# Kernel optimization log

Measured on AMD Instinct MI355X. Metric: run time of the kernel, lower is better.

## Reference

```python
import math
import jax, jax.numpy as jnp
import numpy as np

DIM = 3
NB = 8  # 2**DIM blades, grade-sorted: [1, e1, e2, e3, e12, e13, e23, e123]
GRADE_SLICES = [(0, 1), (1, 4), (4, 7), (7, 8)]
SUBSPACES = [1, 3, 3, 1]
GRADE_IDX = np.repeat(np.arange(4), SUBSPACES)  # blade -> grade index
EPS = 1e-6
SQRT2 = math.sqrt(2.0)


def _build_cayley():
    # Cl(3,0) Euclidean Cayley table, blades sorted by (grade, bitmask).
    masks = sorted(range(NB), key=lambda m: (bin(m).count("1"), m))
    pos = {m: i for i, m in enumerate(masks)}
    cay = np.zeros((NB, NB, NB), dtype=np.float32)
    for i, mi in enumerate(masks):
        for k, mk in enumerate(masks):
            a, s = mi >> 1, 0
            while a:
                s += bin(a & mk).count("1")
                a >>= 1
            cay[i, pos[mi ^ mk], k] = -1.0 if (s & 1) else 1.0
    triples = []
    for gi in range(4):
        for gj in range(4):
            for gk in range(4):
                (i0, i1), (j0, j1), (k0, k1) = GRADE_SLICES[gi], GRADE_SLICES[gj], GRADE_SLICES[gk]
                if np.any(cay[i0:i1, j0:j1, k0:k1] != 0):
                    triples.append((gi, gj, gk))
    return cay, triples

CAYLEY_NP, TRIPLES = _build_cayley()
NPATHS = len(TRIPLES)  # 20 nonzero grade-triple paths for Cl(3,0)


def mv_linear(x, w, b=None):
    # x: [B,n,8]; w: [m,n,4] (one weight per grade subspace); bias -> scalar blade only.
    w8 = w[..., GRADE_IDX]  # [m,n,8]
    out = jnp.einsum("bni,mni->bmi", x, w8)
    if b is not None:
        out = out.at[..., 0].add(b)
    return out


def grade_q(x):
    # per-grade squared magnitude (Euclidean metric -> all blade signs +1): [B,n,8]->[B,n,4]
    return jnp.stack([jnp.sum(x[..., s:e] ** 2, axis=-1) for s, e in GRADE_SLICES], axis=-1)


def normalization(x, a):
    # CGENN NormalizationLayer (init=0): interpolate per-grade norm toward 1 via sigmoid gate.
    norms = jnp.sqrt(grade_q(x))  # [B,n,4]
    sa = jax.nn.sigmoid(a)  # [n,4]
    norms = sa[None] * (norms - 1.0) + 1.0
    return x / (norms[..., GRADE_IDX] + EPS)


def mv_silu(x, a, b):
    # MVSiLU with invariant='mag2': gate on [scalar, q_grade1, q_grade2, q_grade3].
    q = grade_q(x)  # [B,n,4]
    inv = jnp.concatenate([x[..., :1], q[..., 1:]], axis=-1)  # [B,n,4]
    gate = a[None] * inv + b[None]
    return jax.nn.sigmoid(gate[..., GRADE_IDX]) * x


def fc_geometric_product(x, xr, w, cayley):
    # out[b,m,j] = sum_{n,i,k} x[b,n,i] * cayley[i,j,k] * W[m,n,path(gi,gj,gk)] * xr[b,n,k]
    B, n = x.shape[0], x.shape[1]
    m = w.shape[0]
    out = jnp.zeros((B, m, NB), dtype=x.dtype)
    for t, (gi, gj, gk) in enumerate(TRIPLES):
        (i0, i1), (j0, j1), (k0, k1) = GRADE_SLICES[gi], GRADE_SLICES[gj], GRADE_SLICES[gk]
        tmp = jnp.einsum("bni,ijk,bnk->bnj", x[..., i0:i1], cayley[i0:i1, j0:j1, k0:k1], xr[..., k0:k1])
        out = out.at[:, :, j0:j1].add(jnp.einsum("bnj,mn->bmj", tmp, w[:, :, t]))
    return out


def cw_geometric_product(x, xr, w, cayley):
    # channel-wise steerable GP: out[b,n,j] = sum_{i,k} x[b,n,i]*cayley[i,j,k]*w[n,path]*xr[b,n,k]
    out = jnp.zeros_like(x)
    for t, (gi, gj, gk) in enumerate(TRIPLES):
        (i0, i1), (j0, j1), (k0, k1) = GRADE_SLICES[gi], GRADE_SLICES[gj], GRADE_SLICES[gk]
        tmp = jnp.einsum("bni,ijk,bnk->bnj", x[..., i0:i1], cayley[i0:i1, j0:j1, k0:k1], xr[..., k0:k1])
        out = out.at[:, :, j0:j1].add(tmp * w[None, :, t, None])
    return out


B, IN, HID, OUT = 1024, 256, 512, 128


def setup_inputs():
    key = jax.random.key(0)
    ks = jax.random.split(key, 16)

    def nrm(k, shape, std):
        return jax.random.normal(k, shape, dtype=jnp.float32) * std

    s_in = 1.0 / math.sqrt(IN)
    s_hid = 1.0 / math.sqrt(HID)
    return {
        "x": jax.random.normal(ks[0], (B, IN, NB), dtype=jnp.float32),
        "lr1_w": nrm(ks[1], (IN, IN, 4), s_in),
        "n1_a": jnp.zeros((IN, 4), jnp.float32),
        "ll1_w": nrm(ks[2], (HID, IN, 4), s_in),
        "ll1_b": jnp.zeros((HID,), jnp.float32),
        "w1": nrm(ks[3], (HID, IN, NPATHS), 1.0 / math.sqrt(IN * (DIM + 1))),
        "act_a": jnp.ones((HID, 4), jnp.float32),
        "act_b": jnp.zeros((HID, 4), jnp.float32),
        "lrg_w": nrm(ks[4], (HID, HID, 4), s_hid),
        "ng_a": jnp.zeros((HID, 4), jnp.float32),
        "llg_w": nrm(ks[5], (HID, HID, 4), s_hid),
        "llg_b": jnp.zeros((HID,), jnp.float32),
        "wg": nrm(ks[6], (HID, NPATHS), 1.0 / math.sqrt(DIM + 1)),
        "lr2_w": nrm(ks[7], (HID, HID, 4), s_hid),
        "n2_a": jnp.zeros((HID, 4), jnp.float32),
        "ll2_w": nrm(ks[8], (OUT, HID, 4), s_hid),
        "ll2_b": jnp.zeros((OUT,), jnp.float32),
        "w2": nrm(ks[9], (OUT, HID, NPATHS), 1.0 / math.sqrt(HID * (DIM + 1))),
    }


def reference(x, lr1_w, n1_a, ll1_w, ll1_b, w1, act_a, act_b,
              lrg_w, ng_a, llg_w, llg_b, wg,
              lr2_w, n2_a, ll2_w, ll2_b, w2):
    cayley = jnp.asarray(CAYLEY_NP)
    # fcgp1: right linear -> normalize -> weighted geometric product + first-order term
    xr = normalization(mv_linear(x, lr1_w), n1_a)
    h = (mv_linear(x, ll1_w, ll1_b) + fc_geometric_product(x, xr, w1, cayley)) / SQRT2
    h = mv_silu(h, act_a, act_b)
    # channel-wise steerable geometric product layer
    hr = normalization(mv_linear(h, lrg_w), ng_a)
    h = (mv_linear(h, llg_w, llg_b) + cw_geometric_product(h, hr, wg, cayley)) / SQRT2
    h = mv_silu(h, act_a, act_b)
    # fcgp2
    hr = normalization(mv_linear(h, lr2_w), n2_a)
    out = (mv_linear(h, ll2_w, ll2_b) + fc_geometric_product(h, hr, w2, cayley)) / SQRT2
    return out
```

## Files before the change

kernel.cpp:

```cpp
#include <hip/hip_runtime.h>
#include <math.h>


typedef unsigned short u16;
typedef __attribute__((ext_vector_type(8))) short short8;
typedef __attribute__((ext_vector_type(4))) float f32x4;

#define RSQRT2F 0.70710678118654752440f

__device__ inline void gl_lds16(const void* g, void* l) {
  __builtin_amdgcn_global_load_lds(
      (const __attribute__((address_space(1))) void*)g,
      (__attribute__((address_space(3))) void*)l, 16, 0, 0);
}

__device__ constexpr int PP_I[64] = {
  0,0,0,0,0,0,0,0,  1,1,1,1,1,1,1,1,  2,2,2,2,2,2,2,2,  3,3,3,3,3,3,3,3,
  4,4,4,4,4,4,4,4,  5,5,5,5,5,5,5,5,  6,6,6,6,6,6,6,6,  7,7,7,7,7,7,7,7};
__device__ constexpr int PP_K[64] = {
  0,1,2,3,4,5,6,7,  0,1,2,3,4,5,6,7,  0,1,2,3,4,5,6,7,  0,1,2,3,4,5,6,7,
  0,1,2,3,4,5,6,7,  0,1,2,3,4,5,6,7,  0,1,2,3,4,5,6,7,  0,1,2,3,4,5,6,7};
__device__ constexpr int PP_C[64] = {
   0, 1, 2, 3, 4, 5, 6, 7,
   9, 8,15,16,13,14,21,20,
  10,15, 8,17,12,21,14,19,
  11,16,17, 8,21,12,13,18,
  29,24,23,35,22,34,33,28,
  30,25,35,23,34,22,32,27,
  31,35,25,24,33,32,22,26,
  43,42,41,40,39,38,37,36};
__device__ constexpr int PP_T[64] = {
   0, 1, 1, 1, 2, 2, 2, 3,
   5, 4, 7, 7, 6, 6, 9, 8,
   5, 7, 4, 7, 6, 9, 6, 8,
   5, 7, 7, 4, 9, 6, 6, 8,
  13,11,11,15,10,14,14,12,
  13,11,15,11,14,10,14,12,
  13,15,11,11,14,14,10,12,
  19,18,18,18,17,17,17,16};
__device__ constexpr int PP_J[64] = {
  0,1,2,3,4,5,6,7,
  1,0,4,5,2,3,7,6,
  2,4,0,6,1,7,3,5,
  3,5,6,0,7,1,2,4,
  4,2,1,7,0,6,5,3,
  5,3,7,1,6,0,4,2,
  6,7,3,2,5,4,0,1,
  7,6,5,4,3,2,1,0};
__device__ constexpr float PP_S[64] = {
  1, 1, 1, 1, 1, 1, 1, 1,
  1, 1, 1, 1, 1, 1, 1, 1,
  1,-1, 1, 1,-1,-1, 1,-1,
  1,-1,-1, 1, 1,-1,-1, 1,
  1,-1, 1, 1,-1,-1, 1,-1,
  1,-1,-1, 1, 1,-1,-1, 1,
  1, 1,-1, 1,-1, 1,-1,-1,
  1, 1,-1, 1,-1, 1,-1,-1};

__device__ constexpr int GJ_CNT[8] = {4,6,6,6,6,6,6,4};
__device__ constexpr int GJ_C[8][6] = {
  {0,8,22,36,0,0},
  {1,9,12,23,26,37},
  {2,10,13,24,27,38},
  {3,11,14,25,28,39},
  {4,15,18,29,32,40},
  {5,16,19,30,33,41},
  {6,17,20,31,34,42},
  {7,21,35,43,0,0}};
__device__ constexpr int GJ_T[8][6] = {
  {0,4,10,16,0,0},
  {1,5,6,11,12,17},
  {1,5,6,11,12,17},
  {1,5,6,11,12,17},
  {2,7,8,13,14,18},
  {2,7,8,13,14,18},
  {2,7,8,13,14,18},
  {3,9,15,19,0,0}};
__device__ constexpr int GRADE[8] = {0,1,1,1,2,2,2,3};

__device__ inline float sigm(float x) { return 1.0f / (1.0f + expf(-x)); }
__device__ inline u16 f2bf(float f) {
  unsigned u = __float_as_uint(f);
  return (u16)((u + 0x7fffu + ((u >> 16) & 1u)) >> 16);
}
__device__ inline float bf2f(u16 h) { return __uint_as_float(((unsigned)h) << 16); }

#define BT 128
#define MT 128
#define BKc 64

__global__ __launch_bounds__(256) void mfma_gemm(
    const u16* __restrict__ Alin, const u16* __restrict__ Pfeat,
    const u16* __restrict__ WLin, const u16* __restrict__ WLin2,
    const u16* __restrict__ WGp,
    float* __restrict__ out1, float* __restrict__ out2,
    int N, int M, int aug, int planeA, int planeO, int KSbits, int KCbits)
{
  const int zz    = blockIdx.z;
  const int set   = zz >> (3 + KSbits);
  const int rem   = zz & ((8 << KSbits) - 1);
  const int j     = rem >> KSbits;
  const int slice = rem & ((1 << KSbits) - 1);
  const u16* WL   = set ? WLin2 : WLin;
  float* outp     = set ? out2 : out1;

  const int b0   = blockIdx.y * BT;
  const int m0   = blockIdx.x * MT;
  const int tid  = threadIdx.x;
  const int lane = tid & 63;
  const int wave = tid >> 6;
  const int wr   = wave >> 1;
  const int wc   = wave & 1;
  const int l15  = lane & 15;
  const int lq   = lane >> 4;

  __shared__ u16 As[BT * BKc];
  __shared__ u16 Bs[MT * BKc];

  f32x4 zero = {0.f, 0.f, 0.f, 0.f};
  f32x4 acc[4][4];
  #pragma unroll
  for (int r = 0; r < 4; ++r)
    #pragma unroll
    for (int c = 0; c < 4; ++c) acc[r][c] = zero;

  const int g = GRADE[j];
  const int npass = aug ? (1 + GJ_CNT[j]) : 1;
  const int KC = 1 << KCbits;
  const int cper = (npass << KCbits) >> KSbits;
  const int cbeg = slice * cper;

  const int srow = lane >> 3;
  const int sslot = lane & 7;

  for (int ci = cbeg; ci < cbeg + cper; ++ci) {
    const int p  = ci >> KCbits;
    const int k0 = (ci & (KC - 1)) << 6;
    const u16* Abase = (p == 0) ? Alin + (size_t)j * planeA
                                : Pfeat + (size_t)GJ_C[j][p - 1] * planeA;
    const u16* Wbase = (p == 0) ? WL + (size_t)g * M * N
                                : WGp + (size_t)GJ_T[j][p - 1] * M * N;
    const u16* Asrc = Abase + (size_t)b0 * N + k0;
    const u16* Bsrc = Wbase + (size_t)m0 * N + k0;

    __syncthreads();
    #pragma unroll
    for (int q = 0; q < 4; ++q) {
      int inst = wave * 4 + q;
      int row  = inst * 8 + srow;
      int kg   = sslot ^ (row & 7);
      gl_lds16(Asrc + (size_t)row * N + kg * 8, &As[inst * 512]);
    }
    #pragma unroll
    for (int q = 0; q < 4; ++q) {
      int inst = wave * 4 + q;
      int row  = inst * 8 + srow;
      int kg   = sslot ^ (row & 7);
      gl_lds16(Bsrc + (size_t)row * N + kg * 8, &Bs[inst * 512]);
    }
    __syncthreads();

    #pragma unroll
    for (int s = 0; s < 2; ++s) {
      const int kq = s * 4 + lq;
      short8 af[4], bfr[4];
      #pragma unroll
      for (int r = 0; r < 4; ++r) {
        int row = wr * 64 + r * 16 + l15;
        af[r] = *(const short8*)(&As[row * BKc + (kq ^ (row & 7)) * 8]);
      }
      #pragma unroll
      for (int c = 0; c < 4; ++c) {
        int row = wc * 64 + c * 16 + l15;
        bfr[c] = *(const short8*)(&Bs[row * BKc + (kq ^ (row & 7)) * 8]);
      }
      #pragma unroll
      for (int r = 0; r < 4; ++r)
        #pragma unroll
        for (int c = 0; c < 4; ++c)
          acc[r][c] = __builtin_amdgcn_mfma_f32_16x16x32_bf16(af[r], bfr[c], acc[r][c], 0, 0, 0);
    }
  }

  float* obase = outp + (size_t)(slice * 8 + j) * planeO;
  #pragma unroll
  for (int r = 0; r < 4; ++r)
    #pragma unroll
    for (int c = 0; c < 4; ++c)
      #pragma unroll
      for (int e = 0; e < 4; ++e) {
        int bb = b0 + wr * 64 + r * 16 + lq * 4 + e;
        int mm = m0 + wc * 64 + c * 16 + l15;
        obase[(size_t)bb * M + mm] = acc[r][c][e];
      }
}

struct RepackDesc { const float* in; u16* out; int MN; int S; };
struct RepackArgs { RepackDesc d[8]; const float* x; u16* xp; int PS; };

__global__ void repack_all(RepackArgs a)
{
  int mn = blockIdx.x * 256 + threadIdx.x;
  if (blockIdx.y == 8) {
    if (mn >= a.PS) return;
    float v[8];
    *(float4*)(v)     = *(const float4*)(a.x + (size_t)mn * 8);
    *(float4*)(v + 4) = *(const float4*)(a.x + (size_t)mn * 8 + 4);
    #pragma unroll
    for (int jj = 0; jj < 8; ++jj) a.xp[(size_t)jj * a.PS + mn] = f2bf(v[jj]);
    return;
  }
  RepackDesc d = a.d[blockIdx.y];
  if (mn >= d.MN) return;
  if (d.S == 4) {
    float4 v = ((const float4*)d.in)[mn];
    d.out[(size_t)0 * d.MN + mn] = f2bf(v.x);
    d.out[(size_t)1 * d.MN + mn] = f2bf(v.y);
    d.out[(size_t)2 * d.MN + mn] = f2bf(v.z);
    d.out[(size_t)3 * d.MN + mn] = f2bf(v.w);
  } else {
    #pragma unroll
    for (int q = 0; q < 5; ++q) {
      float4 v = *(const float4*)(d.in + (size_t)mn * 20 + q * 4);
      d.out[(size_t)(q * 4 + 0) * d.MN + mn] = f2bf(v.x);
      d.out[(size_t)(q * 4 + 1) * d.MN + mn] = f2bf(v.y);
      d.out[(size_t)(q * 4 + 2) * d.MN + mn] = f2bf(v.z);
      d.out[(size_t)(q * 4 + 3) * d.MN + mn] = f2bf(v.w);
    }
  }
}

__global__ void pair_norm_p(const u16* __restrict__ up, const float* __restrict__ vpart,
                            const float* __restrict__ na, u16* __restrict__ Pp,
                            int PS, int M, int KS)
{
  int t = blockIdx.x * 256 + threadIdx.x;
  if (t >= PS) return;
  int m = t % M;
  float u[8], v[8];
  #pragma unroll
  for (int jj = 0; jj < 8; ++jj) {
    u[jj] = bf2f(up[(size_t)jj * PS + t]);
    float s = 0.f;
    for (int sl = 0; sl < KS; ++sl) s += vpart[(size_t)(sl * 8 + jj) * PS + t];
    v[jj] = s;
  }
  float q[4];
  q[0] = sqrtf(v[0] * v[0]);
  q[1] = sqrtf(v[1] * v[1] + v[2] * v[2] + v[3] * v[3]);
  q[2] = sqrtf(v[4] * v[4] + v[5] * v[5] + v[6] * v[6]);
  q[3] = sqrtf(v[7] * v[7]);
  float sc[4];
  #pragma unroll
  for (int gg = 0; gg < 4; ++gg) {
    float sa = sigm(na[m * 4 + gg]);
    sc[gg] = 1.0f / (sa * (q[gg] - 1.0f) + 1.0f + 1e-6f);
  }
  #pragma unroll
  for (int jj = 0; jj < 8; ++jj) v[jj] *= sc[GRADE[jj]];
  float p[44];
  #pragma unroll
  for (int c = 0; c < 44; ++c) p[c] = 0.f;
  #pragma unroll
  for (int e = 0; e < 64; ++e)
    p[PP_C[e]] += PP_S[e] * u[PP_I[e]] * v[PP_K[e]];
  #pragma unroll
  for (int c = 0; c < 44; ++c) Pp[(size_t)c * PS + t] = f2bf(p[c]);
}

__global__ void bias_silu_p(const float* __restrict__ hpart, const float* __restrict__ bias,
                            const float* __restrict__ ga, const float* __restrict__ gb,
                            u16* __restrict__ sh, int PS, int M, int KS)
{
  int t = blockIdx.x * 256 + threadIdx.x;
  if (t >= PS) return;
  int m = t % M;
  float v[8];
  #pragma unroll
  for (int jj = 0; jj < 8; ++jj) {
    float s = 0.f;
    for (int sl = 0; sl < KS; ++sl) s += hpart[(size_t)(sl * 8 + jj) * PS + t];
    v[jj] = s;
  }
  v[0] += bias[m];
  #pragma unroll
  for (int jj = 0; jj < 8; ++jj) v[jj] *= RSQRT2F;
  float inv[4];
  inv[0] = v[0];
  inv[1] = v[1]*v[1] + v[2]*v[2] + v[3]*v[3];
  inv[2] = v[4]*v[4] + v[5]*v[5] + v[6]*v[6];
  inv[3] = v[7]*v[7];
  float gt[4];
  #pragma unroll
  for (int gg = 0; gg < 4; ++gg)
    gt[gg] = sigm(ga[m * 4 + gg] * inv[gg] + gb[m * 4 + gg]);
  #pragma unroll
  for (int jj = 0; jj < 8; ++jj)
    sh[(size_t)jj * PS + t] = f2bf(v[jj] * gt[GRADE[jj]]);
}

__global__ void cw_silu_p(const float* __restrict__ llg, const u16* __restrict__ up,
                          const float* __restrict__ hrraw, const float* __restrict__ na,
                          const float* __restrict__ wg, const float* __restrict__ bias,
                          const float* __restrict__ ga, const float* __restrict__ gb,
                          u16* __restrict__ sh, int PS, int M)
{
  int t = blockIdx.x * 256 + threadIdx.x;
  if (t >= PS) return;
  int n = t % M;
  float acc[8], u[8], v[8], w[20];
  #pragma unroll
  for (int jj = 0; jj < 8; ++jj) {
    acc[jj] = llg[(size_t)jj * PS + t];
    u[jj]   = bf2f(up[(size_t)jj * PS + t]);
    v[jj]   = hrraw[(size_t)jj * PS + t];
  }
  float q[4];
  q[0] = sqrtf(v[0] * v[0]);
  q[1] = sqrtf(v[1] * v[1] + v[2] * v[2] + v[3] * v[3]);
  q[2] = sqrtf(v[4] * v[4] + v[5] * v[5] + v[6] * v[6]);
  q[3] = sqrtf(v[7] * v[7]);
  float sc[4];
  #pragma unroll
  for (int gg = 0; gg < 4; ++gg) {
    float sa = sigm(na[n * 4 + gg]);
    sc[gg] = 1.0f / (sa * (q[gg] - 1.0f) + 1.0f + 1e-6f);
  }
  #pragma unroll
  for (int jj = 0; jj < 8; ++jj) v[jj] *= sc[GRADE[jj]];
  #pragma unroll
  for (int qq = 0; qq < 5; ++qq)
    *(float4*)(w + qq * 4) = *(const float4*)(wg + (size_t)n * 20 + qq * 4);
  acc[0] += bias[n];
  #pragma unroll
  for (int e = 0; e < 64; ++e)
    acc[PP_J[e]] += PP_S[e] * u[PP_I[e]] * v[PP_K[e]] * w[PP_T[e]];
  #pragma unroll
  for (int jj = 0; jj < 8; ++jj) acc[jj] *= RSQRT2F;
  float inv[4];
  inv[0] = acc[0];
  inv[1] = acc[1]*acc[1] + acc[2]*acc[2] + acc[3]*acc[3];
  inv[2] = acc[4]*acc[4] + acc[5]*acc[5] + acc[6]*acc[6];
  inv[3] = acc[7]*acc[7];
  float gt[4];
  #pragma unroll
  for (int gg = 0; gg < 4; ++gg)
    gt[gg] = sigm(ga[n * 4 + gg] * inv[gg] + gb[n * 4 + gg]);
  #pragma unroll
  for (int jj = 0; jj < 8; ++jj)
    sh[(size_t)jj * PS + t] = f2bf(acc[jj] * gt[GRADE[jj]]);
}

__global__ void final_p(const float* __restrict__ pre, const float* __restrict__ bias,
                        float* __restrict__ outp, int PS, int M, int KS)
{
  int t = blockIdx.x * 256 + threadIdx.x;
  if (t >= PS) return;
  int m = t % M;
  float v[8];
  #pragma unroll
  for (int jj = 0; jj < 8; ++jj) {
    float s = 0.f;
    for (int sl = 0; sl < KS; ++sl) s += pre[(size_t)(sl * 8 + jj) * PS + t];
    v[jj] = s;
  }
  v[0] += bias[m];
  #pragma unroll
  for (int jj = 0; jj < 8; ++jj) v[jj] *= RSQRT2F;
  *(float4*)(outp + (size_t)t * 8)     = *(float4*)(v);
  *(float4*)(outp + (size_t)t * 8 + 4) = *(float4*)(v + 4);
}

extern "C" void kernel_launch(void* const* d_in, const int* in_sizes, int n_in,
                              void* d_out, int out_size, void* d_ws, size_t ws_size,
                              hipStream_t stream)
{
  const float* x     = (const float*)d_in[0];
  const float* lr1_w = (const float*)d_in[1];
  const float* n1_a  = (const float*)d_in[2];
  const float* ll1_w = (const float*)d_in[3];
  const float* ll1_b = (const float*)d_in[4];
  const float* w1    = (const float*)d_in[5];
  const float* act_a = (const float*)d_in[6];
  const float* act_b = (const float*)d_in[7];
  const float* lrg_w = (const float*)d_in[8];
  const float* ng_a  = (const float*)d_in[9];
  const float* llg_w = (const float*)d_in[10];
  const float* llg_b = (const float*)d_in[11];
  const float* wg    = (const float*)d_in[12];
  const float* lr2_w = (const float*)d_in[13];
  const float* n2_a  = (const float*)d_in[14];
  const float* ll2_w = (const float*)d_in[15];
  const float* ll2_b = (const float*)d_in[16];
  const float* w2    = (const float*)d_in[17];
  float* out = (float*)d_out;

  u16* W = (u16*)d_ws;
  size_t o = 0;
  u16* WL1  = W + o; o +=  262144;
  u16* WLL1 = W + o; o +=  524288;
  u16* WG1  = W + o; o += 2621440;
  u16* WLRG = W + o; o += 1048576;
  u16* WLLG = W + o; o += 1048576;
  u16* WLR2 = W + o; o += 1048576;
  u16* WLL2 = W + o; o +=  262144;
  u16* WG2  = W + o; o += 1310720;
  u16* XB   = W + o; o += 2097152;
  u16* HB   = W + o; o += 4194304;
  u16* P    = W + o; o += 23068672;
  float* f1 = (float*)(W + o);
  float* f2 = f1 + 8388608;
  float* hrP  = f2;
  float* llgP = f2 + 4194304;

  dim3 blk(256);
  const int PS1 = 1024 * 256, PS2 = 1024 * 512, PSO = 1024 * 128;

  RepackArgs ra = {{
    {lr1_w, WL1, 65536, 4}, {ll1_w, WLL1, 131072, 4}, {w1, WG1, 131072, 20},
    {lrg_w, WLRG, 262144, 4}, {llg_w, WLLG, 262144, 4}, {lr2_w, WLR2, 262144, 4},
    {ll2_w, WLL2, 65536, 4}, {w2, WG2, 65536, 20}},
    x, XB, PS1};
  repack_all<<<dim3(1024, 9), blk, 0, stream>>>(ra);

  mfma_gemm<<<dim3(2, 8, 16), blk, 0, stream>>>(XB, nullptr, WL1, nullptr, nullptr,
      f1, nullptr, 256, 256, 0, PS1, PS1, 1, 2);
  pair_norm_p<<<PS1 / 256, blk, 0, stream>>>(XB, f1, n1_a, P, PS1, 256, 2);
  mfma_gemm<<<dim3(4, 8, 16), blk, 0, stream>>>(XB, P, WLL1, nullptr, WG1,
      f1, nullptr, 256, 512, 1, PS1, PS2, 1, 2);
  bias_silu_p<<<PS2 / 256, blk, 0, stream>>>(f1, ll1_b, act_a, act_b, HB, PS2, 512, 2);

  mfma_gemm<<<dim3(4, 8, 16), blk, 0, stream>>>(HB, nullptr, WLRG, WLLG, nullptr,
      hrP, llgP, 512, 512, 0, PS2, PS2, 0, 3);
  cw_silu_p<<<PS2 / 256, blk, 0, stream>>>(llgP, HB, hrP, ng_a, wg, llg_b, act_a, act_b,
      HB, PS2, 512);

  mfma_gemm<<<dim3(4, 8, 16), blk, 0, stream>>>(HB, nullptr, WLR2, nullptr, nullptr,
      f1, nullptr, 512, 512, 0, PS2, PS2, 1, 3);
  pair_norm_p<<<PS2 / 256, blk, 0, stream>>>(HB, f1, n2_a, P, PS2, 512, 2);
  mfma_gemm<<<dim3(1, 8, 64), blk, 0, stream>>>(HB, P, WLL2, nullptr, WG2,
      f1, nullptr, 512, 128, 1, PS2, PSO, 3, 3);
  final_p<<<PSO / 256, blk, 0, stream>>>(f1, ll2_b, out, PSO, 128, 8);
}
```

Measured before the change: 261.8 us.

## Template GEMM tile shape and store intermediate partial sums in bf16

Templates the MFMA GEMM on block tile and wave layout, moving most launches to 256x128 tiles with four waves stacked along rows. The intermediate outputs (split-K partials, hr/llg projections) are now written as bf16 instead of fp32, and the consumer kernels convert them back. This halves the intermediate write and read traffic and improves reuse of weight tiles. In exchange, split-K partial sums are rounded to bf16 before being added, which loses precision, and the larger tiles mean fewer blocks and more registers per wave.

Result: slower. 268.4 us (+2.5%).

```diff
diff --git a/kernel.cpp b/kernel.cpp
--- a/kernel.cpp
+++ b/kernel.cpp
@@ -85,32 +85,36 @@
 }
 __device__ inline float bf2f(u16 h) { return __uint_as_float(((unsigned)h) << 16); }
 
-#define BT 128
-#define MT 128
 #define BKc 64
 
+template<int BT, int MT, int WR, int WC, int OUT16>
 __global__ __launch_bounds__(256) void mfma_gemm(
     const u16* __restrict__ Alin, const u16* __restrict__ Pfeat,
     const u16* __restrict__ WLin, const u16* __restrict__ WLin2,
     const u16* __restrict__ WGp,
-    float* __restrict__ out1, float* __restrict__ out2,
+    void* __restrict__ out1, void* __restrict__ out2,
     int N, int M, int aug, int planeA, int planeO, int KSbits, int KCbits)
 {
+  constexpr int FR = BT / 16 / WR;
+  constexpr int FC = MT / 16 / WC;
+  constexpr int AI = BT / 32;
+  constexpr int BI = MT / 32;
+
   const int zz    = blockIdx.z;
   const int set   = zz >> (3 + KSbits);
   const int rem   = zz & ((8 << KSbits) - 1);
   const int j     = rem >> KSbits;
   const int slice = rem & ((1 << KSbits) - 1);
   const u16* WL   = set ? WLin2 : WLin;
-  float* outp     = set ? out2 : out1;
+  void* outp      = set ? out2 : out1;
 
   const int b0   = blockIdx.y * BT;
   const int m0   = blockIdx.x * MT;
   const int tid  = threadIdx.x;
   const int lane = tid & 63;
   const int wave = tid >> 6;
-  const int wr   = wave >> 1;
-  const int wc   = wave & 1;
+  const int wr   = wave / WC;
+  const int wc   = wave % WC;
   const int l15  = lane & 15;
   const int lq   = lane >> 4;
 
@@ -118,11 +122,11 @@
   __shared__ u16 Bs[MT * BKc];
 
   f32x4 zero = {0.f, 0.f, 0.f, 0.f};
-  f32x4 acc[4][4];
-  #pragma unroll
-  for (int r = 0; r < 4; ++r)
-    #pragma unroll
-    for (int c = 0; c < 4; ++c) acc[r][c] = zero;
+  f32x4 acc[FR][FC];
+  #pragma unroll
+  for (int r = 0; r < FR; ++r)
+    #pragma unroll
+    for (int c = 0; c < FC; ++c) acc[r][c] = zero;
 
   const int g = GRADE[j];
   const int npass = aug ? (1 + GJ_CNT[j]) : 1;
@@ -130,7 +134,7 @@
   const int cper = (npass << KCbits) >> KSbits;
   const int cbeg = slice * cper;
 
-  const int srow = lane >> 3;
+  const int srow  = lane >> 3;
   const int sslot = lane & 7;
 
   for (int ci = cbeg; ci < cbeg + cper; ++ci) {
@@ -145,15 +149,15 @@
 
     __syncthreads();
     #pragma unroll
-    for (int q = 0; q < 4; ++q) {
-      int inst = wave * 4 + q;
+    for (int q = 0; q < AI; ++q) {
+      int inst = wave * AI + q;
       int row  = inst * 8 + srow;
       int kg   = sslot ^ (row & 7);
       gl_lds16(Asrc + (size_t)row * N + kg * 8, &As[inst * 512]);
     }
     #pragma unroll
-    for (int q = 0; q < 4; ++q) {
-      int inst = wave * 4 + q;
+    for (int q = 0; q < BI; ++q) {
+      int inst = wave * BI + q;
       int row  = inst * 8 + srow;
       int kg   = sslot ^ (row & 7);
       gl_lds16(Bsrc + (size_t)row * N + kg * 8, &Bs[inst * 512]);
@@ -163,35 +167,36 @@
     #pragma unroll
     for (int s = 0; s < 2; ++s) {
       const int kq = s * 4 + lq;
-      short8 af[4], bfr[4];
+      short8 af[FR], bfr[FC];
       #pragma unroll
-      for (int r = 0; r < 4; ++r) {
-        int row = wr * 64 + r * 16 + l15;
+      for (int r = 0; r < FR; ++r) {
+        int row = wr * (FR * 16) + r * 16 + l15;
         af[r] = *(const short8*)(&As[row * BKc + (kq ^ (row & 7)) * 8]);
       }
       #pragma unroll
-      for (int c = 0; c < 4; ++c) {
-        int row = wc * 64 + c * 16 + l15;
+      for (int c = 0; c < FC; ++c) {
+        int row = wc * (FC * 16) + c * 16 + l15;
         bfr[c] = *(const short8*)(&Bs[row * BKc + (kq ^ (row & 7)) * 8]);
       }
       #pragma unroll
-      for (int r = 0; r < 4; ++r)
+      for (int r = 0; r < FR; ++r)
         #pragma unroll
-        for (int c = 0; c < 4; ++c)
+        for (int c = 0; c < FC; ++c)
           acc[r][c] = __builtin_amdgcn_mfma_f32_16x16x32_bf16(af[r], bfr[c], acc[r][c], 0, 0, 0);
     }
   }
 
-  float* obase = outp + (size_t)(slice * 8 + j) * planeO;
-  #pragma unroll
-  for (int r = 0; r < 4; ++r)
-    #pragma unroll
-    for (int c = 0; c < 4; ++c)
+  const size_t po = (size_t)(slice * 8 + j) * planeO;
+  #pragma unroll
+  for (int r = 0; r < FR; ++r)
+    #pragma unroll
+    for (int c = 0; c < FC; ++c)
       #pragma unroll
       for (int e = 0; e < 4; ++e) {
-        int bb = b0 + wr * 64 + r * 16 + lq * 4 + e;
-        int mm = m0 + wc * 64 + c * 16 + l15;
-        obase[(size_t)bb * M + mm] = acc[r][c][e];
+        int bb = b0 + wr * (FR * 16) + r * 16 + lq * 4 + e;
+        int mm = m0 + wc * (FC * 16) + c * 16 + l15;
+        if (OUT16) ((u16*)outp)[po + (size_t)bb * M + mm] = f2bf(acc[r][c][e]);
+        else       ((float*)outp)[po + (size_t)bb * M + mm] = acc[r][c][e];
       }
 }
 
@@ -230,7 +235,7 @@
   }
 }
 
-__global__ void pair_norm_p(const u16* __restrict__ up, const float* __restrict__ vpart,
+__global__ void pair_norm_p(const u16* __restrict__ up, const u16* __restrict__ vpart,
                             const float* __restrict__ na, u16* __restrict__ Pp,
                             int PS, int M, int KS)
 {
@@ -242,7 +247,7 @@
   for (int jj = 0; jj < 8; ++jj) {
     u[jj] = bf2f(up[(size_t)jj * PS + t]);
     float s = 0.f;
-    for (int sl = 0; sl < KS; ++sl) s += vpart[(size_t)(sl * 8 + jj) * PS + t];
+    for (int sl = 0; sl < KS; ++sl) s += bf2f(vpart[(size_t)(sl * 8 + jj) * PS + t]);
     v[jj] = s;
   }
   float q[4];
@@ -268,7 +273,7 @@
   for (int c = 0; c < 44; ++c) Pp[(size_t)c * PS + t] = f2bf(p[c]);
 }
 
-__global__ void bias_silu_p(const float* __restrict__ hpart, const float* __restrict__ bias,
+__global__ void bias_silu_p(const u16* __restrict__ hpart, const float* __restrict__ bias,
                             const float* __restrict__ ga, const float* __restrict__ gb,
                             u16* __restrict__ sh, int PS, int M, int KS)
 {
@@ -279,7 +284,7 @@
   #pragma unroll
   for (int jj = 0; jj < 8; ++jj) {
     float s = 0.f;
-    for (int sl = 0; sl < KS; ++sl) s += hpart[(size_t)(sl * 8 + jj) * PS + t];
+    for (int sl = 0; sl < KS; ++sl) s += bf2f(hpart[(size_t)(sl * 8 + jj) * PS + t]);
     v[jj] = s;
   }
   v[0] += bias[m];
@@ -299,8 +304,8 @@
     sh[(size_t)jj * PS + t] = f2bf(v[jj] * gt[GRADE[jj]]);
 }
 
-__global__ void cw_silu_p(const float* __restrict__ llg, const u16* __restrict__ up,
-                          const float* __restrict__ hrraw, const float* __restrict__ na,
+__global__ void cw_silu_p(const u16* __restrict__ llg, const u16* __restrict__ up,
+                          const u16* __restrict__ hrraw, const float* __restrict__ na,
                           const float* __restrict__ wg, const float* __restrict__ bias,
                           const float* __restrict__ ga, const float* __restrict__ gb,
                           u16* __restrict__ sh, int PS, int M)
@@ -311,9 +316,9 @@
   float acc[8], u[8], v[8], w[20];
   #pragma unroll
   for (int jj = 0; jj < 8; ++jj) {
-    acc[jj] = llg[(size_t)jj * PS + t];
+    acc[jj] = bf2f(llg[(size_t)jj * PS + t]);
     u[jj]   = bf2f(up[(size_t)jj * PS + t]);
-    v[jj]   = hrraw[(size_t)jj * PS + t];
+    v[jj]   = bf2f(hrraw[(size_t)jj * PS + t]);
   }
   float q[4];
   q[0] = sqrtf(v[0] * v[0]);
@@ -408,10 +413,11 @@
   u16* XB   = W + o; o += 2097152;
   u16* HB   = W + o; o += 4194304;
   u16* P    = W + o; o += 23068672;
+  u16* PB16 = W + o; o += 8388608;
+  u16* HRG  = W + o; o += 8388608;
+  u16* hr16  = HRG;
+  u16* llg16 = HRG + 4194304;
   float* f1 = (float*)(W + o);
-  float* f2 = f1 + 8388608;
-  float* hrP  = f2;
-  float* llgP = f2 + 4194304;
 
   dim3 blk(256);
   const int PS1 = 1024 * 256, PS2 = 1024 * 512, PSO = 1024 * 128;
@@ -423,22 +429,27 @@
     x, XB, PS1};
   repack_all<<<dim3(1024, 9), blk, 0, stream>>>(ra);
 
-  mfma_gemm<<<dim3(2, 8, 16), blk, 0, stream>>>(XB, nullptr, WL1, nullptr, nullptr,
-      f1, nullptr, 256, 256, 0, PS1, PS1, 1, 2);
-  pair_norm_p<<<PS1 / 256, blk, 0, stream>>>(XB, f1, n1_a, P, PS1, 256, 2);
-  mfma_gemm<<<dim3(4, 8, 16), blk, 0, stream>>>(XB, P, WLL1, nullptr, WG1,
-      f1, nullptr, 256, 512, 1, PS1, PS2, 1, 2);
-  bias_silu_p<<<PS2 / 256, blk, 0, stream>>>(f1, ll1_b, act_a, act_b, HB, PS2, 512, 2);
-
-  mfma_gemm<<<dim3(4, 8, 16), blk, 0, stream>>>(HB, nullptr, WLRG, WLLG, nullptr,
-      hrP, llgP, 512, 512, 0, PS2, PS2, 0, 3);
-  cw_silu_p<<<PS2 / 256, blk, 0, stream>>>(llgP, HB, hrP, ng_a, wg, llg_b, act_a, act_b,
+  mfma_gemm<128,128,2,2,1><<<dim3(2, 8, 16), blk, 0, stream>>>(
+      XB, nullptr, WL1, nullptr, nullptr, PB16, nullptr,
+      256, 256, 0, PS1, PS1, 1, 2);
+  pair_norm_p<<<PS1 / 256, blk, 0, stream>>>(XB, PB16, n1_a, P, PS1, 256, 2);
+  mfma_gemm<256,128,4,1,1><<<dim3(4, 4, 16), blk, 0, stream>>>(
+      XB, P, WLL1, nullptr, WG1, PB16, nullptr,
+      256, 512, 1, PS1, PS2, 1, 2);
+  bias_silu_p<<<PS2 / 256, blk, 0, stream>>>(PB16, ll1_b, act_a, act_b, HB, PS2, 512, 2);
+
+  mfma_gemm<256,128,4,1,1><<<dim3(4, 4, 16), blk, 0, stream>>>(
+      HB, nullptr, WLRG, WLLG, nullptr, hr16, llg16,
+      512, 512, 0, PS2, PS2, 0, 3);
+  cw_silu_p<<<PS2 / 256, blk, 0, stream>>>(llg16, HB, hr16, ng_a, wg, llg_b, act_a, act_b,
       HB, PS2, 512);
 
-  mfma_gemm<<<dim3(4, 8, 16), blk, 0, stream>>>(HB, nullptr, WLR2, nullptr, nullptr,
-      f1, nullptr, 512, 512, 0, PS2, PS2, 1, 3);
-  pair_norm_p<<<PS2 / 256, blk, 0, stream>>>(HB, f1, n2_a, P, PS2, 512, 2);
-  mfma_gemm<<<dim3(1, 8, 64), blk, 0, stream>>>(HB, P, WLL2, nullptr, WG2,
-      f1, nullptr, 512, 128, 1, PS2, PSO, 3, 3);
+  mfma_gemm<256,128,4,1,1><<<dim3(4, 4, 16), blk, 0, stream>>>(
+      HB, nullptr, WLR2, nullptr, nullptr, PB16, nullptr,
+      512, 512, 0, PS2, PS2, 1, 3);
+  pair_norm_p<<<PS2 / 256, blk, 0, stream>>>(HB, PB16, n2_a, P, PS2, 512, 2);
+  mfma_gemm<256,128,4,1,0><<<dim3(1, 4, 64), blk, 0, stream>>>(
+      HB, P, WLL2, nullptr, WG2, f1, nullptr,
+      512, 128, 1, PS2, PSO, 3, 3);
   final_p<<<PSO / 256, blk, 0, stream>>>(f1, ll2_b, out, PSO, 128, 8);
 }
```

## Double-buffer LDS tiles with async global_load_lds prefetch in GEMM loop

Applied to the files above, without the earlier changes.

Converts the single-buffered K-loop into a two-stage pipeline: the next chunk's A and B tiles are issued via global_load_lds into the alternate LDS buffer before computing on the current one. It waits with a manual vmcnt(8) plus barrier so only the current tile's loads must complete. This hides global-to-LDS latency behind MFMA work, at the cost of doubling LDS usage (possible occupancy reduction) and relying on hand-written waitcnt correctness.

New measurement: 258.3 us. Within noise of the previous version (-1.3%).

```diff
diff --git a/kernel.cpp b/kernel.cpp
--- a/kernel.cpp
+++ b/kernel.cpp
@@ -114,8 +114,8 @@
   const int l15  = lane & 15;
   const int lq   = lane >> 4;
 
-  __shared__ u16 As[BT * BKc];
-  __shared__ u16 Bs[MT * BKc];
+  __shared__ u16 AsB[2][BT * BKc];
+  __shared__ u16 BsB[2][MT * BKc];
 
   f32x4 zero = {0.f, 0.f, 0.f, 0.f};
   f32x4 acc[4][4];
@@ -130,36 +130,65 @@
   const int cper = (npass << KCbits) >> KSbits;
   const int cbeg = slice * cper;
 
-  const int srow = lane >> 3;
+  const int srow  = lane >> 3;
   const int sslot = lane & 7;
 
-  for (int ci = cbeg; ci < cbeg + cper; ++ci) {
+  {
+    const int ci = cbeg;
     const int p  = ci >> KCbits;
     const int k0 = (ci & (KC - 1)) << 6;
-    const u16* Abase = (p == 0) ? Alin + (size_t)j * planeA
-                                : Pfeat + (size_t)GJ_C[j][p - 1] * planeA;
-    const u16* Wbase = (p == 0) ? WL + (size_t)g * M * N
-                                : WGp + (size_t)GJ_T[j][p - 1] * M * N;
-    const u16* Asrc = Abase + (size_t)b0 * N + k0;
-    const u16* Bsrc = Wbase + (size_t)m0 * N + k0;
-
-    __syncthreads();
+    const u16* Ab = (p == 0) ? Alin + (size_t)j * planeA
+                             : Pfeat + (size_t)GJ_C[j][p - 1] * planeA;
+    const u16* Wb = (p == 0) ? WL + (size_t)g * M * N
+                             : WGp + (size_t)GJ_T[j][p - 1] * (size_t)M * N;
+    const u16* As0 = Ab + (size_t)b0 * N + k0;
+    const u16* Bs0 = Wb + (size_t)m0 * N + k0;
     #pragma unroll
     for (int q = 0; q < 4; ++q) {
-      int inst = wave * 4 + q;
-      int row  = inst * 8 + srow;
-      int kg   = sslot ^ (row & 7);
-      gl_lds16(Asrc + (size_t)row * N + kg * 8, &As[inst * 512]);
+      int inst = wave * 4 + q, row = inst * 8 + srow;
+      int kg = sslot ^ (row & 7);
+      gl_lds16(As0 + (size_t)row * N + kg * 8, &AsB[0][inst * 512]);
     }
     #pragma unroll
     for (int q = 0; q < 4; ++q) {
-      int inst = wave * 4 + q;
-      int row  = inst * 8 + srow;
-      int kg   = sslot ^ (row & 7);
-      gl_lds16(Bsrc + (size_t)row * N + kg * 8, &Bs[inst * 512]);
+      int inst = wave * 4 + q, row = inst * 8 + srow;
+      int kg = sslot ^ (row & 7);
+      gl_lds16(Bs0 + (size_t)row * N + kg * 8, &BsB[0][inst * 512]);
     }
-    __syncthreads();
-
+  }
+
+  #pragma unroll 1
+  for (int ci = cbeg; ci < cbeg + cper; ++ci) {
+    const int buf = (ci - cbeg) & 1;
+    if (ci + 1 < cbeg + cper) {
+      const int cn = ci + 1;
+      const int p  = cn >> KCbits;
+      const int k0 = (cn & (KC - 1)) << 6;
+      const u16* Ab = (p == 0) ? Alin + (size_t)j * planeA
+                               : Pfeat + (size_t)GJ_C[j][p - 1] * planeA;
+      const u16* Wb = (p == 0) ? WL + (size_t)g * M * N
+                               : WGp + (size_t)GJ_T[j][p - 1] * (size_t)M * N;
+      const u16* As1 = Ab + (size_t)b0 * N + k0;
+      const u16* Bs1 = Wb + (size_t)m0 * N + k0;
+      #pragma unroll
+      for (int q = 0; q < 4; ++q) {
+        int inst = wave * 4 + q, row = inst * 8 + srow;
+        int kg = sslot ^ (row & 7);
+        gl_lds16(As1 + (size_t)row * N + kg * 8, &AsB[1 - buf][inst * 512]);
+      }
+      #pragma unroll
+      for (int q = 0; q < 4; ++q) {
+        int inst = wave * 4 + q, row = inst * 8 + srow;
+        int kg = sslot ^ (row & 7);
+        gl_lds16(Bs1 + (size_t)row * N + kg * 8, &BsB[1 - buf][inst * 512]);
+      }
+      asm volatile("s_waitcnt vmcnt(8)\n\ts_barrier" ::: "memory");
+    } else {
+      asm volatile("s_waitcnt vmcnt(0)\n\ts_barrier" ::: "memory");
+    }
+
+    const u16* As = &AsB[buf][0];
+    const u16* Bs = &BsB[buf][0];
     #pragma unroll
     for (int s = 0; s < 2; ++s) {
       const int kq = s * 4 + lq;
@@ -180,6 +209,7 @@
         for (int c = 0; c < 4; ++c)
           acc[r][c] = __builtin_amdgcn_mfma_f32_16x16x32_bf16(af[r], bfr[c], acc[r][c], 0, 0, 0);
     }
+    asm volatile("s_barrier" ::: "memory");
   }
 
   float* obase = outp + (size_t)(slice * 8 + j) * planeO;
```
